# Optimization experiments

Hardware: AMD Instinct MI355X
Metric: run time of the kernel (lower is better)

The kernel has to match this reference:

```python
import jax, jax.numpy as jnp
import numpy as np

THRESHOLD = 0.0
B = 4_194_304


def setup_inputs() -> dict:
    key = jax.random.key(0)
    ks = jax.random.split(key, 20)
    s = 0.1  # small init scale
    inp = {
        "data": jax.random.normal(ks[0], (B, 1, 2, 2), dtype=jnp.float32),
        # ConvFilter: Conv2d(1,1,kernel=2) -> weight (1,2,2) (in-ch, kh, kw), scalar bias
        "conv_w": jax.random.normal(ks[1], (1, 2, 2), dtype=jnp.float32) * s,
        "conv_b": jax.random.normal(ks[2], (), dtype=jnp.float32) * s,
        # QCNN linear layers, stored as (in, out)
        "W_fm": jax.random.normal(ks[3], (8, 16), dtype=jnp.float32) * s,
        "b_fm": jax.random.normal(ks[4], (16,), dtype=jnp.float32) * s,
        "W_c1": jax.random.normal(ks[5], (16, 16), dtype=jnp.float32) * s,
        "b_c1": jax.random.normal(ks[6], (16,), dtype=jnp.float32) * s,
        "W_p1": jax.random.normal(ks[7], (16, 12), dtype=jnp.float32) * s,
        "b_p1": jax.random.normal(ks[8], (12,), dtype=jnp.float32) * s,
        "W_c2": jax.random.normal(ks[9], (12, 8), dtype=jnp.float32) * s,
        "b_c2": jax.random.normal(ks[10], (8,), dtype=jnp.float32) * s,
        "W_p2": jax.random.normal(ks[11], (8, 4), dtype=jnp.float32) * s,
        "b_p2": jax.random.normal(ks[12], (4,), dtype=jnp.float32) * s,
        "W_c3": jax.random.normal(ks[13], (4, 4), dtype=jnp.float32) * s,
        "b_c3": jax.random.normal(ks[14], (4,), dtype=jnp.float32) * s,
        "W_h": jax.random.normal(ks[15], (4, 1), dtype=jnp.float32) * s,
        "b_h": jax.random.normal(ks[16], (1,), dtype=jnp.float32) * s,
    }
    return inp


def reference(data, conv_w, conv_b, W_fm, b_fm, W_c1, b_c1, W_p1, b_p1,
              W_c2, b_c2, W_p2, b_p2, W_c3, b_c3, W_h, b_h):
    # ConvFilter on a 2x2 patch: conv output is a single 1x1 logit per sample,
    # so the mean over activations is just sigmoid(logit - threshold).
    logit = jnp.einsum('bchw,chw->b', data, conv_w) + conv_b  # [B]
    conv_val = jax.nn.sigmoid(logit - THRESHOLD)              # [B]
    # Replicate scalar to the 8-dim QCNN input.
    x = jnp.broadcast_to(conv_val[:, None], (data.shape[0], 8))
    x = jnp.tanh(x @ W_fm + b_fm)   # [B,16]
    x = jnp.tanh(x @ W_c1 + b_c1)   # [B,16]
    x = jnp.tanh(x @ W_p1 + b_p1)   # [B,12]
    x = jnp.tanh(x @ W_c2 + b_c2)   # [B,8]
    x = jnp.tanh(x @ W_p2 + b_p2)   # [B,4]
    x = jnp.tanh(x @ W_c3 + b_c3)   # [B,4]
    return jax.nn.sigmoid(x @ W_h + b_h)  # [B,1]
```

## Files before the change

kernel.cpp:

```cpp
#include <hip/hip_runtime.h>
#include <math.h>

#define NLUT 256

typedef float f32x4 __attribute__((ext_vector_type(4)));

__device__ __forceinline__ float fast_tanh(float x) {
    float e = __expf(2.0f * x);
    return __fdividef(e - 1.0f, e + 1.0f);
}

__device__ __forceinline__ float eval_net(
    float x,
    const float* W_fm, const float* b_fm,
    const float* W_c1, const float* b_c1,
    const float* W_p1, const float* b_p1,
    const float* W_c2, const float* b_c2,
    const float* W_p2, const float* b_p2,
    const float* W_c3, const float* b_c3,
    const float* W_h,  const float* b_h)
{
    float h[16], g[16];
    #pragma unroll
    for (int j = 0; j < 16; ++j) {
        float a = b_fm[j];
        #pragma unroll
        for (int i = 0; i < 8; ++i) a = fmaf(x, W_fm[i * 16 + j], a);
        h[j] = fast_tanh(a);
    }
    #pragma unroll
    for (int j = 0; j < 16; ++j) {
        float a = b_c1[j];
        #pragma unroll
        for (int i = 0; i < 16; ++i) a = fmaf(h[i], W_c1[i * 16 + j], a);
        g[j] = fast_tanh(a);
    }
    #pragma unroll
    for (int j = 0; j < 12; ++j) {
        float a = b_p1[j];
        #pragma unroll
        for (int i = 0; i < 16; ++i) a = fmaf(g[i], W_p1[i * 12 + j], a);
        h[j] = fast_tanh(a);
    }
    #pragma unroll
    for (int j = 0; j < 8; ++j) {
        float a = b_c2[j];
        #pragma unroll
        for (int i = 0; i < 12; ++i) a = fmaf(h[i], W_c2[i * 8 + j], a);
        g[j] = fast_tanh(a);
    }
    #pragma unroll
    for (int j = 0; j < 4; ++j) {
        float a = b_p2[j];
        #pragma unroll
        for (int i = 0; i < 8; ++i) a = fmaf(g[i], W_p2[i * 4 + j], a);
        h[j] = fast_tanh(a);
    }
    #pragma unroll
    for (int j = 0; j < 4; ++j) {
        float a = b_c3[j];
        #pragma unroll
        for (int i = 0; i < 4; ++i) a = fmaf(h[i], W_c3[i * 4 + j], a);
        g[j] = fast_tanh(a);
    }
    float a = b_h[0];
    #pragma unroll
    for (int i = 0; i < 4; ++i) a = fmaf(g[i], W_h[i], a);
    return __fdividef(1.0f, 1.0f + __expf(-a));
}

__global__ __launch_bounds__(256) void build_lut_kernel(
    const float* __restrict__ W_fm, const float* __restrict__ b_fm,
    const float* __restrict__ W_c1, const float* __restrict__ b_c1,
    const float* __restrict__ W_p1, const float* __restrict__ b_p1,
    const float* __restrict__ W_c2, const float* __restrict__ b_c2,
    const float* __restrict__ W_p2, const float* __restrict__ b_p2,
    const float* __restrict__ W_c3, const float* __restrict__ b_c3,
    const float* __restrict__ W_h,  const float* __restrict__ b_h,
    float* __restrict__ lut)
{
    __shared__ float s[785];
    for (int j = threadIdx.x; j < 128; j += 256) s[j]       = W_fm[j];
    if (threadIdx.x < 16)                        s[128 + threadIdx.x] = b_fm[threadIdx.x];
    for (int j = threadIdx.x; j < 256; j += 256) s[144 + j] = W_c1[j];
    if (threadIdx.x < 16)                        s[400 + threadIdx.x] = b_c1[threadIdx.x];
    for (int j = threadIdx.x; j < 192; j += 256) s[416 + j] = W_p1[j];
    if (threadIdx.x < 12)                        s[608 + threadIdx.x] = b_p1[threadIdx.x];
    for (int j = threadIdx.x; j < 96;  j += 256) s[620 + j] = W_c2[j];
    if (threadIdx.x < 8)                         s[716 + threadIdx.x] = b_c2[threadIdx.x];
    for (int j = threadIdx.x; j < 32;  j += 256) s[724 + j] = W_p2[j];
    if (threadIdx.x < 4)                         s[756 + threadIdx.x] = b_p2[threadIdx.x];
    for (int j = threadIdx.x; j < 16;  j += 256) s[760 + j] = W_c3[j];
    if (threadIdx.x < 4)                         s[776 + threadIdx.x] = b_c3[threadIdx.x];
    if (threadIdx.x < 4)                         s[780 + threadIdx.x] = W_h[threadIdx.x];
    if (threadIdx.x == 0)                        s[784] = b_h[0];
    __syncthreads();

    int i = blockIdx.x * 256 + threadIdx.x;
    if (i > NLUT) return;

    float x = (float)i * (1.0f / (float)NLUT);
    lut[i] = eval_net(x,
                      s + 0,   s + 128, s + 144, s + 400, s + 416, s + 608,
                      s + 620, s + 716, s + 724, s + 756, s + 760, s + 776,
                      s + 780, s + 784);
}

__global__ __launch_bounds__(256) void qcnn_main_kernel(
    const f32x4* __restrict__ data,
    const float* __restrict__ conv_w, const float* __restrict__ conv_b,
    const float* __restrict__ lut, float* __restrict__ out, int n)
{
    const float w0 = conv_w[0], w1 = conv_w[1], w2 = conv_w[2], w3 = conv_w[3];
    const float cb = conv_b[0];

    int tid = blockIdx.x * 256 + threadIdx.x;
    int stride = gridDim.x * 256;
    for (int sidx = tid; sidx < n; sidx += stride) {
        f32x4 d = data[sidx];
        float logit = fmaf(d.x, w0, fmaf(d.y, w1,
                      fmaf(d.z, w2, fmaf(d.w, w3, cb))));
        float cv = __fdividef(1.0f, 1.0f + __expf(-logit));
        float t = cv * (float)NLUT;
        int idx = (int)t;
        idx = idx < NLUT ? idx : (NLUT - 1);
        idx = idx > 0 ? idx : 0;
        float fr = t - (float)idx;
        float v0 = lut[idx];
        float v1 = lut[idx + 1];
        out[sidx] = fmaf(fr, v1 - v0, v0);
    }
}

extern "C" void kernel_launch(void* const* d_in, const int* in_sizes, int n_in,
                              void* d_out, int out_size, void* d_ws, size_t ws_size,
                              hipStream_t stream) {
    const float* data   = (const float*)d_in[0];
    const float* conv_w = (const float*)d_in[1];
    const float* conv_b = (const float*)d_in[2];
    const float* W_fm = (const float*)d_in[3];  const float* b_fm = (const float*)d_in[4];
    const float* W_c1 = (const float*)d_in[5];  const float* b_c1 = (const float*)d_in[6];
    const float* W_p1 = (const float*)d_in[7];  const float* b_p1 = (const float*)d_in[8];
    const float* W_c2 = (const float*)d_in[9];  const float* b_c2 = (const float*)d_in[10];
    const float* W_p2 = (const float*)d_in[11]; const float* b_p2 = (const float*)d_in[12];
    const float* W_c3 = (const float*)d_in[13]; const float* b_c3 = (const float*)d_in[14];
    const float* W_h  = (const float*)d_in[15]; const float* b_h  = (const float*)d_in[16];
    float* out = (float*)d_out;
    const int B = in_sizes[0] / 4;

    float* lut = (float*)d_ws;
    build_lut_kernel<<<(NLUT + 1 + 255) / 256, 256, 0, stream>>>(
        W_fm, b_fm, W_c1, b_c1, W_p1, b_p1, W_c2, b_c2,
        W_p2, b_p2, W_c3, b_c3, W_h, b_h, lut);

    qcnn_main_kernel<<<4096, 256, 0, stream>>>(
        (const f32x4*)data, conv_w, conv_b, lut, out, B);
}
```

Before: 28.00 us.

## Fuse LUT build into main kernel with shared-memory LUT and unrolled loads

Merges the LUT-building kernel and the main streaming kernel into one launch. Each of 256 blocks of 1024 threads rebuilds the 257-entry LUT in shared memory as float2 pairs, so interpolation needs a single LDS read instead of two global reads. The grid-stride loop is unrolled by four to issue more loads in flight. This removes one kernel launch and the global LUT traffic, but every block now runs the 8-16-16-12-8-4-4-1 network for 257 inputs before it can start streaming, and the grid is smaller.

```diff
diff --git a/kernel.cpp b/kernel.cpp
--- a/kernel.cpp
+++ b/kernel.cpp
@@ -69,7 +69,9 @@
     return __fdividef(1.0f, 1.0f + __expf(-a));
 }
 
-__global__ __launch_bounds__(256) void build_lut_kernel(
+__global__ __launch_bounds__(1024) void qcnn_fused_kernel(
+    const f32x4* __restrict__ data,
+    const float* __restrict__ conv_w, const float* __restrict__ conv_b,
     const float* __restrict__ W_fm, const float* __restrict__ b_fm,
     const float* __restrict__ W_c1, const float* __restrict__ b_c1,
     const float* __restrict__ W_p1, const float* __restrict__ b_p1,
@@ -77,58 +79,86 @@
     const float* __restrict__ W_p2, const float* __restrict__ b_p2,
     const float* __restrict__ W_c3, const float* __restrict__ b_c3,
     const float* __restrict__ W_h,  const float* __restrict__ b_h,
-    float* __restrict__ lut)
+    float* __restrict__ out, int n)
 {
-    __shared__ float s[785];
-    for (int j = threadIdx.x; j < 128; j += 256) s[j]       = W_fm[j];
-    if (threadIdx.x < 16)                        s[128 + threadIdx.x] = b_fm[threadIdx.x];
-    for (int j = threadIdx.x; j < 256; j += 256) s[144 + j] = W_c1[j];
-    if (threadIdx.x < 16)                        s[400 + threadIdx.x] = b_c1[threadIdx.x];
-    for (int j = threadIdx.x; j < 192; j += 256) s[416 + j] = W_p1[j];
-    if (threadIdx.x < 12)                        s[608 + threadIdx.x] = b_p1[threadIdx.x];
-    for (int j = threadIdx.x; j < 96;  j += 256) s[620 + j] = W_c2[j];
-    if (threadIdx.x < 8)                         s[716 + threadIdx.x] = b_c2[threadIdx.x];
-    for (int j = threadIdx.x; j < 32;  j += 256) s[724 + j] = W_p2[j];
-    if (threadIdx.x < 4)                         s[756 + threadIdx.x] = b_p2[threadIdx.x];
-    for (int j = threadIdx.x; j < 16;  j += 256) s[760 + j] = W_c3[j];
-    if (threadIdx.x < 4)                         s[776 + threadIdx.x] = b_c3[threadIdx.x];
-    if (threadIdx.x < 4)                         s[780 + threadIdx.x] = W_h[threadIdx.x];
-    if (threadIdx.x == 0)                        s[784] = b_h[0];
+    __shared__ float  s[785];
+    __shared__ float  sv[NLUT + 1];
+    __shared__ float2 lutl[NLUT];
+
+    const int t = threadIdx.x;
+
+    if (t < 128)  s[t]       = W_fm[t];
+    if (t < 16)   s[128 + t] = b_fm[t];
+    if (t < 256)  s[144 + t] = W_c1[t];
+    if (t < 16)   s[400 + t] = b_c1[t];
+    if (t < 192)  s[416 + t] = W_p1[t];
+    if (t < 12)   s[608 + t] = b_p1[t];
+    if (t < 96)   s[620 + t] = W_c2[t];
+    if (t < 8)    s[716 + t] = b_c2[t];
+    if (t < 32)   s[724 + t] = W_p2[t];
+    if (t < 4)    s[756 + t] = b_p2[t];
+    if (t < 16)   s[760 + t] = W_c3[t];
+    if (t < 4)    s[776 + t] = b_c3[t];
+    if (t < 4)    s[780 + t] = W_h[t];
+    if (t == 0)   s[784]     = b_h[0];
     __syncthreads();
 
-    int i = blockIdx.x * 256 + threadIdx.x;
-    if (i > NLUT) return;
+    if (t <= NLUT) {
+        sv[t] = eval_net((float)t * (1.0f / (float)NLUT),
+                         s + 0,   s + 128, s + 144, s + 400, s + 416, s + 608,
+                         s + 620, s + 716, s + 724, s + 756, s + 760, s + 776,
+                         s + 780, s + 784);
+    }
+    __syncthreads();
+    if (t < NLUT) lutl[t] = make_float2(sv[t], sv[t + 1]);
+    __syncthreads();
 
-    float x = (float)i * (1.0f / (float)NLUT);
-    lut[i] = eval_net(x,
-                      s + 0,   s + 128, s + 144, s + 400, s + 416, s + 608,
-                      s + 620, s + 716, s + 724, s + 756, s + 760, s + 776,
-                      s + 780, s + 784);
-}
-
-__global__ __launch_bounds__(256) void qcnn_main_kernel(
-    const f32x4* __restrict__ data,
-    const float* __restrict__ conv_w, const float* __restrict__ conv_b,
-    const float* __restrict__ lut, float* __restrict__ out, int n)
-{
     const float w0 = conv_w[0], w1 = conv_w[1], w2 = conv_w[2], w3 = conv_w[3];
     const float cb = conv_b[0];
 
-    int tid = blockIdx.x * 256 + threadIdx.x;
-    int stride = gridDim.x * 256;
-    for (int sidx = tid; sidx < n; sidx += stride) {
-        f32x4 d = data[sidx];
+    const int tid = blockIdx.x * 1024 + t;
+    const int stride = gridDim.x * 1024;
+
+    int i = tid;
+    for (; i + 3 * stride < n; i += 4 * stride) {
+        f32x4 d0 = data[i];
+        f32x4 d1 = data[i + stride];
+        f32x4 d2 = data[i + 2 * stride];
+        f32x4 d3 = data[i + 3 * stride];
+
+        float r[4];
+        f32x4 dd[4] = {d0, d1, d2, d3};
+        #pragma unroll
+        for (int k = 0; k < 4; ++k) {
+            float logit = fmaf(dd[k].x, w0, fmaf(dd[k].y, w1,
+                          fmaf(dd[k].z, w2, fmaf(dd[k].w, w3, cb))));
+            float cv = __fdividef(1.0f, 1.0f + __expf(-logit));
+            float tt = cv * (float)NLUT;
+            int idx = (int)tt;
+            idx = idx < NLUT ? idx : (NLUT - 1);
+            idx = idx > 0 ? idx : 0;
+            float fr = tt - (float)idx;
+            float2 v = lutl[idx];
+            r[k] = fmaf(fr, v.y - v.x, v.x);
+        }
+
+        out[i]              = r[0];
+        out[i + stride]     = r[1];
+        out[i + 2 * stride] = r[2];
+        out[i + 3 * stride] = r[3];
+    }
+    for (; i < n; i += stride) {
+        f32x4 d = data[i];
         float logit = fmaf(d.x, w0, fmaf(d.y, w1,
                       fmaf(d.z, w2, fmaf(d.w, w3, cb))));
         float cv = __fdividef(1.0f, 1.0f + __expf(-logit));
-        float t = cv * (float)NLUT;
-        int idx = (int)t;
+        float tt = cv * (float)NLUT;
+        int idx = (int)tt;
         idx = idx < NLUT ? idx : (NLUT - 1);
         idx = idx > 0 ? idx : 0;
-        float fr = t - (float)idx;
-        float v0 = lut[idx];
-        float v1 = lut[idx + 1];
-        out[sidx] = fmaf(fr, v1 - v0, v0);
+        float fr = tt - (float)idx;
+        float2 v = lutl[idx];
+        out[i] = fmaf(fr, v.y - v.x, v.x);
     }
 }
 
@@ -148,11 +178,8 @@
     float* out = (float*)d_out;
     const int B = in_sizes[0] / 4;
 
-    float* lut = (float*)d_ws;
-    build_lut_kernel<<<(NLUT + 1 + 255) / 256, 256, 0, stream>>>(
+    qcnn_fused_kernel<<<256, 1024, 0, stream>>>(
+        (const f32x4*)data, conv_w, conv_b,
         W_fm, b_fm, W_c1, b_c1, W_p1, b_p1, W_c2, b_c2,
-        W_p2, b_p2, W_c3, b_c3, W_h, b_h, lut);
-
-    qcnn_main_kernel<<<4096, 256, 0, stream>>>(
-        (const f32x4*)data, conv_w, conv_b, lut, out, B);
+        W_p2, b_p2, W_c3, b_c3, W_h, b_h, out, B);
 }
```

After: 28.38 us. Within noise of the previous version (+1.4%).
